# Kernel optimization log

Hardware: AMD Instinct MI355X
Metric: run time of the kernel (lower is better)

## Reference

```python
import jax, jax.numpy as jnp
import numpy as np

B, C, W, H = 1024, 1, 128, 128
NUM_IDS = 64
MARGIN = 0.3


def setup_inputs() -> dict:
    key = jax.random.key(0)
    k1, k2 = jax.random.split(key)
    inputs = jax.random.normal(k1, (B, C, W, H), dtype=jnp.float32)
    targets = jax.random.randint(k2, (B,), 0, NUM_IDS, dtype=jnp.int32)
    return {"inputs": inputs, "targets": targets}


def _dc_align(anchor, other):
    # Batched cross-attention alignment (DCModuleOptimized assumption):
    # modi = softmax(anchor @ other^T / sqrt(h)) @ other, per sample.
    h = anchor.shape[-1]
    scale = 1.0 / jnp.sqrt(jnp.asarray(h, anchor.dtype))
    att = jax.nn.softmax(jnp.einsum('bij,bkj->bik', anchor, other) * scale, axis=-1)
    return jnp.einsum('bik,bkj->bij', att, other)


def reference(inputs, targets):
    b, c, w, h = inputs.shape
    x = inputs.reshape(b, -1)                      # (n, d); requires c == 1 downstream
    n = b
    # Pairwise Euclidean distances, stable clamp as in torch code
    sq = jnp.sum(x * x, axis=1)                    # (n,)
    dist = sq[:, None] + sq[None, :] - 2.0 * (x @ x.T)
    dist = jnp.sqrt(jnp.clip(dist, 1e-12, None))   # (n, n)
    mask = targets[:, None] == targets[None, :]    # (n, n) same-identity mask
    # Vectorized hard mining (replaces the per-row Python loop)
    NEG = jnp.asarray(-1e30, dist.dtype)
    POS = jnp.asarray(1e30, dist.dtype)
    hp_idx = jnp.argmax(jnp.where(mask, dist, NEG), axis=1)   # hardest positive per row
    hn_idx = jnp.argmin(jnp.where(mask, POS, dist), axis=1)   # hardest negative per row
    anchor = x.reshape(b, w, h)
    h_pos = anchor[hp_idx]                         # (b, w, h) gathered hard positives
    h_neg = anchor[hn_idx]                         # (b, w, h) gathered hard negatives
    # DC module applied over the whole batch at once
    modi_pos = _dc_align(anchor, h_pos)
    modi_neg = _dc_align(anchor, h_neg)
    dap = anchor.reshape(b, -1) - modi_pos.reshape(b, -1)
    dan = anchor.reshape(b, -1) - modi_neg.reshape(b, -1)
    dist_ap = jnp.sqrt(jnp.sum(dap * dap, axis=1))
    dist_an = jnp.sqrt(jnp.sum(dan * dan, axis=1))
    # MarginRankingLoss with y = 1: mean(relu(dist_ap - dist_an + margin))
    loss = jnp.mean(jax.nn.relu(dist_ap - dist_an + MARGIN))
    return loss
```

## Files before the change

kernel.cpp:

```cpp
#include <hip/hip_runtime.h>
#include <stdint.h>

#define NSAMP 1024
#define D 16384
#define WH 128
#define MARGIN 0.3f
#define SCALE 0.08838834764831845f
#define RSCALE 11.313708498984761f
#define MARG 0.03f
#define NKS 16
#define NTILE 36

typedef unsigned int uint;
typedef unsigned short ushort_t;

typedef __attribute__((ext_vector_type(8))) short bf16x8;
typedef __attribute__((ext_vector_type(4))) float f32x4;

__device__ __forceinline__ float bf2f(unsigned short b) {
    return __uint_as_float(((uint)b) << 16);
}
__device__ __forceinline__ unsigned short f2bf(float f) {
    uint u = __float_as_uint(f);
    u += 0x7fffu + ((u >> 16) & 1u);
    return (unsigned short)(u >> 16);
}
__device__ __forceinline__ void gload_lds16(const void* g, void* l) {
    __builtin_amdgcn_global_load_lds(
        (const __attribute__((address_space(1))) uint32_t*)g,
        (__attribute__((address_space(3))) uint32_t*)l, 16, 0, 0);
}
__device__ __forceinline__ int lds_off(int row, int col) {
    return row * 256 + ((((col >> 3) ^ (row & 15)) << 4) | ((col & 7) << 1));
}

__global__ __launch_bounds__(256) void k_norms_hi(const float* __restrict__ x,
                                                  float* __restrict__ sq,
                                                  ushort_t* __restrict__ xhi) {
    int b = blockIdx.x;
    int tid = threadIdx.x;
    const float* xr = x + (size_t)b * D;
    ushort_t* hr = xhi + (size_t)b * D;
    float s = 0.f;
    #pragma unroll
    for (int m = 0; m < 16; ++m) {
        int e = m * 1024 + tid * 4;
        float4 v = *(const float4*)(xr + e);
        s += v.x * v.x + v.y * v.y + v.z * v.z + v.w * v.w;
        ushort4 h;
        h.x = f2bf(v.x); h.y = f2bf(v.y); h.z = f2bf(v.z); h.w = f2bf(v.w);
        *(ushort4*)(hr + e) = h;
    }
    for (int off = 32; off; off >>= 1) s += __shfl_down(s, off, 64);
    __shared__ float red[4];
    if ((tid & 63) == 0) red[tid >> 6] = s;
    __syncthreads();
    if (tid == 0) sq[b] = red[0] + red[1] + red[2] + red[3];
}

__global__ __launch_bounds__(256) void k_gram_hi(const ushort_t* __restrict__ xhi,
                                                 float* __restrict__ Gp) {
    int ks = blockIdx.x;
    int t = blockIdx.y;
    int bi = 0, rem = t;
    while (rem >= 8 - bi) { rem -= 8 - bi; ++bi; }
    int bj = bi + rem;
    int i0 = bi * 128, j0 = bj * 128;
    int kstart = ks * (D / NKS);

    int tid = threadIdx.x;
    int w = tid >> 6, lane = tid & 63;
    int wm = w & 1, wn = w >> 1;
    int quad = lane >> 4, m16 = lane & 15;
    int srow = lane >> 2, sseg = lane & 3;
    int swseg = sseg ^ ((srow >> 1) & 3);
    int rsw = (quad ^ ((m16 >> 1) & 3)) << 3;

    __shared__ __align__(16) ushort_t A_s[2][128 * 32];
    __shared__ __align__(16) ushort_t B_s[2][128 * 32];

    f32x4 acc[4][4];
    #pragma unroll
    for (int ii = 0; ii < 4; ++ii)
        #pragma unroll
        for (int jj = 0; jj < 4; ++jj)
            acc[ii][jj] = (f32x4){0.f, 0.f, 0.f, 0.f};

    const size_t Abase = (size_t)i0 * D;
    const size_t Bbase = (size_t)j0 * D;

    auto stage = [&](int bsel, int k0) {
        #pragma unroll
        for (int c = 0; c < 2; ++c) {
            int r = w * 32 + c * 16 + srow;
            size_t go = (size_t)r * D + k0 + swseg * 8;
            int lo = (w * 32 + c * 16) * 32;
            gload_lds16(xhi + Abase + go, &A_s[bsel][lo]);
            gload_lds16(xhi + Bbase + go, &B_s[bsel][lo]);
        }
    };

    stage(0, kstart);
    __syncthreads();
    int buf = 0;
    const int niter = (D / NKS) / 32;
    for (int kb = 0; kb < niter; ++kb) {
        if (kb < niter - 1) stage(buf ^ 1, kstart + (kb + 1) * 32);
        bf16x8 ah[4], bh[4];
        #pragma unroll
        for (int ii = 0; ii < 4; ++ii) {
            int ar = wm * 64 + ii * 16 + m16;
            ah[ii] = *(const bf16x8*)&A_s[buf][ar * 32 + rsw];
        }
        #pragma unroll
        for (int jj = 0; jj < 4; ++jj) {
            int br = wn * 64 + jj * 16 + m16;
            bh[jj] = *(const bf16x8*)&B_s[buf][br * 32 + rsw];
        }
        #pragma unroll
        for (int ii = 0; ii < 4; ++ii)
            #pragma unroll
            for (int jj = 0; jj < 4; ++jj)
                acc[ii][jj] = __builtin_amdgcn_mfma_f32_16x16x32_bf16(ah[ii], bh[jj], acc[ii][jj], 0, 0, 0);
        __syncthreads();
        buf ^= 1;
    }

    float* Gb = Gp + ((size_t)(t * NKS + ks) << 14);
    #pragma unroll
    for (int ii = 0; ii < 4; ++ii)
        #pragma unroll
        for (int jj = 0; jj < 4; ++jj) {
            int rg = wm * 64 + ii * 16 + quad * 4;
            int cg = wn * 64 + jj * 16 + m16;
            #pragma unroll
            for (int r = 0; r < 4; ++r)
                Gb[(rg + r) * 128 + cg] = acc[ii][jj][r];
        }
}

__global__ __launch_bounds__(256) void k_fold_tri(const float* __restrict__ Gp,
                                                  float* __restrict__ G) {
    int t = blockIdx.x;
    int panel = blockIdx.y;
    int bi = 0, rem = t;
    while (rem >= 8 - bi) { rem -= 8 - bi; ++bi; }
    int bj = bi + rem;
    bool diag = (bi == bj);
    int tid = threadIdx.x;

    const float* P = Gp + (((size_t)t * NKS) << 14) + panel * 4096;

    float4 s[4];
    #pragma unroll
    for (int m = 0; m < 4; ++m)
        s[m] = *(const float4*)(P + (tid + 256 * m) * 4);
    #pragma unroll
    for (int p = 1; p < NKS; ++p) {
        const float* Pp = P + (((size_t)p) << 14);
        #pragma unroll
        for (int m = 0; m < 4; ++m) {
            float4 v = *(const float4*)(Pp + (tid + 256 * m) * 4);
            s[m].x += v.x; s[m].y += v.y; s[m].z += v.z; s[m].w += v.w;
        }
    }

    int i0 = bi * 128, j0 = bj * 128, r0 = panel * 32;
    __shared__ float ts[32][129];
    #pragma unroll
    for (int m = 0; m < 4; ++m) {
        int p4 = (tid + 256 * m) * 4;
        int lr = p4 >> 7, lc = p4 & 127;
        *(float4*)(&G[(size_t)(i0 + r0 + lr) * NSAMP + j0 + lc]) = s[m];
        if (!diag) {
            ts[lr][lc] = s[m].x; ts[lr][lc + 1] = s[m].y;
            ts[lr][lc + 2] = s[m].z; ts[lr][lc + 3] = s[m].w;
        }
    }
    if (diag) return;
    __syncthreads();
    int oc = tid >> 1, half = tid & 1;
    float4 o[4];
    #pragma unroll
    for (int k = 0; k < 4; ++k) {
        int rr = half * 16 + k * 4;
        o[k].x = ts[rr][oc]; o[k].y = ts[rr + 1][oc];
        o[k].z = ts[rr + 2][oc]; o[k].w = ts[rr + 3][oc];
    }
    float* Gm = &G[(size_t)(j0 + oc) * NSAMP + i0 + r0 + half * 16];
    #pragma unroll
    for (int k = 0; k < 4; ++k) *(float4*)(Gm + k * 4) = o[k];
}

__global__ __launch_bounds__(256) void k_select_fix(const float* __restrict__ G,
                                                    const float* __restrict__ sq,
                                                    const int* __restrict__ tgt,
                                                    const float* __restrict__ x,
                                                    const ushort_t* __restrict__ xhi,
                                                    int* __restrict__ hp,
                                                    int* __restrict__ hn,
                                                    float* __restrict__ dsq) {
    int i = blockIdx.x;
    int tid = threadIdx.x;
    float sqi = sq[i];
    int ti = tgt[i];
    float dloc[4]; bool sloc[4];
    float pv = -3.0e38f; int pj = 0x7FFFFFFF;
    float nv = 3.0e38f;  int nj = 0x7FFFFFFF;
    #pragma unroll
    for (int m = 0; m < 4; ++m) {
        int j = tid + 256 * m;
        float g = G[(size_t)i * NSAMP + j];
        float d = sqrtf(fmaxf(sqi + sq[j] - 2.f * g, 1e-12f));
        bool same = (tgt[j] == ti);
        dloc[m] = d; sloc[m] = same;
        float cp = same ? d : -1e30f;
        float cn = same ? 1e30f : d;
        if (cp > pv || (cp == pv && j < pj)) { pv = cp; pj = j; }
        if (cn < nv || (cn == nv && j < nj)) { nv = cn; nj = j; }
    }
    for (int off = 32; off; off >>= 1) {
        float opv = __shfl_down(pv, off, 64); int opj = __shfl_down(pj, off, 64);
        float onv = __shfl_down(nv, off, 64); int onj = __shfl_down(nj, off, 64);
        if (opv > pv || (opv == pv && opj < pj)) { pv = opv; pj = opj; }
        if (onv < nv || (onv == nv && onj < nj)) { nv = onv; nj = onj; }
    }
    __shared__ float spv[4], snv[4];
    __shared__ int spj[4], snj[4];
    __shared__ float bb[2];
    __shared__ int cc[2];
    if ((tid & 63) == 0) { int wv = tid >> 6; spv[wv] = pv; spj[wv] = pj; snv[wv] = nv; snj[wv] = nj; }
    __syncthreads();
    if (tid == 0) {
        for (int wv = 1; wv < 4; ++wv) {
            if (spv[wv] > pv || (spv[wv] == pv && spj[wv] < pj)) { pv = spv[wv]; pj = spj[wv]; }
            if (snv[wv] < nv || (snv[wv] == nv && snj[wv] < nj)) { nv = snv[wv]; nj = snj[wv]; }
        }
        hp[i] = pj; hn[i] = nj;
        dsq[i] = sqi; dsq[NSAMP + i] = sqi;
        bb[0] = pv; bb[1] = nv;
        cc[0] = 0; cc[1] = 0;
    }
    __syncthreads();
    {
        int lp = 0, ln = 0;
        #pragma unroll
        for (int m = 0; m < 4; ++m) {
            if (sloc[m] && dloc[m] >= bb[0] - MARG) lp++;
            if (!sloc[m] && dloc[m] <= bb[1] + MARG) ln++;
        }
        if (lp) atomicAdd(&cc[0], lp);
        if (ln) atomicAdd(&cc[1], ln);
    }
    __syncthreads();

    __shared__ int cand[32];
    __shared__ int ncand;
    __shared__ float bred[4];
    const float* xi = x + (size_t)i * D;
    const ushort_t* hi = xhi + (size_t)i * D;
    for (int type = 0; type < 2; ++type) {
        if (cc[type] <= 1) continue;
        if (tid == 0) ncand = 0;
        __syncthreads();
        float bd = bb[type];
        #pragma unroll
        for (int m = 0; m < 4; ++m) {
            int j = tid + 256 * m;
            bool fl = (type == 0) ? (sloc[m] && dloc[m] >= bd - MARG)
                                  : (!sloc[m] && dloc[m] <= bd + MARG);
            if (fl) { int k = atomicAdd(&ncand, 1); if (k < 32) cand[k] = j; }
        }
        __syncthreads();
        int nc = ncand < 32 ? ncand : 32;
        float bestv = (type == 0) ? -3.0e38f : 3.0e38f;
        int bestj = 0x7FFFFFFF;
        for (int c = 0; c < nc; ++c) {
            int j = cand[c];
            const float* xj = x + (size_t)j * D;
            const ushort_t* hj = xhi + (size_t)j * D;
            float corr = 0.f;
            #pragma unroll
            for (int m = 0; m < 16; ++m) {
                int k = m * 1024 + tid * 4;
                float4 xa = *(const float4*)(xi + k);
                float4 xb = *(const float4*)(xj + k);
                ushort4 ha = *(const ushort4*)(hi + k);
                ushort4 hb = *(const ushort4*)(hj + k);
                float a0 = bf2f(ha.x), a1 = bf2f(ha.y), a2 = bf2f(ha.z), a3 = bf2f(ha.w);
                float b0 = bf2f(hb.x), b1 = bf2f(hb.y), b2 = bf2f(hb.z), b3 = bf2f(hb.w);
                corr += a0 * (xb.x - b0) + (xa.x - a0) * b0;
                corr += a1 * (xb.y - b1) + (xa.y - a1) * b1;
                corr += a2 * (xb.z - b2) + (xa.z - a2) * b2;
                corr += a3 * (xb.w - b3) + (xa.w - a3) * b3;
            }
            for (int off = 32; off; off >>= 1) corr += __shfl_down(corr, off, 64);
            if ((tid & 63) == 0) bred[tid >> 6] = corr;
            __syncthreads();
            float cs = bred[0] + bred[1] + bred[2] + bred[3];
            float g = G[(size_t)i * NSAMP + j];
            float d2 = sqi + sq[j] - 2.f * (g + cs);
            float d = sqrtf(fmaxf(d2, 1e-12f));
            if (type == 0) {
                if (d > bestv || (d == bestv && j < bestj)) { bestv = d; bestj = j; }
            } else {
                if (d < bestv || (d == bestv && j < bestj)) { bestv = d; bestj = j; }
            }
            __syncthreads();
        }
        if (tid == 0 && nc > 0) { if (type == 0) hp[i] = bestj; else hn[i] = bestj; }
        __syncthreads();
    }
}

__global__ __launch_bounds__(256) void k_dc_mfma(const ushort_t* __restrict__ xhi,
                                                 const int* __restrict__ hp,
                                                 const int* __restrict__ hn,
                                                 float* __restrict__ dsq) {
    int b = blockIdx.x;
    int which = blockIdx.y;
    int q = blockIdx.z;
    int oidx = (which == 0) ? hp[b] : hn[b];
    const ushort_t* Ag = xhi + (size_t)b * D;
    const ushort_t* Og = xhi + (size_t)oidx * D;

    __shared__ __align__(16) char smem[32768];

    int tid = threadIdx.x;
    int wv = tid >> 6, lane = tid & 63;
    int quad = lane >> 4, m16 = lane & 15;
    int rt = q * 4 + wv;

    bf16x8 af[4];
    #pragma unroll
    for (int ks = 0; ks < 4; ++ks)
        af[ks] = *(const bf16x8*)(Ag + (rt * 16 + m16) * WH + ks * 32 + quad * 8);

    {
        uint4 stg[8];
        #pragma unroll
        for (int k = 0; k < 8; ++k)
            stg[k] = *(const uint4*)((const char*)Og + (size_t)(tid + 256 * k) * 16);
        #pragma unroll
        for (int k = 0; k < 8; ++k) {
            int g = tid + 256 * k;
            *(uint4*)(smem + lds_off(g >> 4, (g & 15) * 8)) = stg[k];
        }
    }
    __syncthreads();

    f32x4 acc[8];
    #pragma unroll
    for (int ti = 0; ti < 8; ++ti)
        acc[ti] = (f32x4){0.f, 0.f, 0.f, 0.f};
    #pragma unroll
    for (int ks = 0; ks < 4; ++ks) {
        bf16x8 of[8];
        #pragma unroll
        for (int ti = 0; ti < 8; ++ti)
            of[ti] = *(const bf16x8*)(smem + lds_off(ti * 16 + m16, (ks * 4 + quad) * 8));
        #pragma unroll
        for (int ti = 0; ti < 8; ++ti)
            acc[ti] = __builtin_amdgcn_mfma_f32_16x16x32_bf16(of[ti], af[ks], acc[ti], 0, 0, 0);
    }

    int c0 = (tid & 31) * 4, h0 = (tid >> 5) * 16;
    uint4 trd[4][2];
    #pragma unroll
    for (int j = 0; j < 4; ++j)
        #pragma unroll
        for (int k = 0; k < 2; ++k)
            trd[j][k] = *(const uint4*)(smem + lds_off(c0 + j, h0 + 8 * k));
    __syncthreads();

    #pragma unroll
    for (int i = 0; i < 16; ++i) {
        uint v[4];
        #pragma unroll
        for (int j = 0; j < 4; ++j) {
            uint wo = ((const uint*)&trd[j][i >> 3])[(i >> 1) & 3];
            v[j] = (i & 1) ? (wo >> 16) : (wo & 0xffffu);
        }
        uint2 pk;
        pk.x = v[0] | (v[1] << 16);
        pk.y = v[2] | (v[3] << 16);
        *(uint2*)(smem + lds_off(h0 + i, c0)) = pk;
    }

    float tpart = 0.f;
    bf16x8 pf[4];
    {
        float mx = -3.0e38f;
        #pragma unroll
        for (int ti = 0; ti < 8; ++ti)
            #pragma unroll
            for (int r = 0; r < 4; ++r) {
                float s = acc[ti][r] * SCALE;
                acc[ti][r] = s;
                mx = fmaxf(mx, s);
            }
        mx = fmaxf(mx, __shfl_xor(mx, 16, 64));
        mx = fmaxf(mx, __shfl_xor(mx, 32, 64));
        float sum = 0.f, tnum = 0.f;
        #pragma unroll
        for (int ti = 0; ti < 8; ++ti)
            #pragma unroll
            for (int r = 0; r < 4; ++r) {
                float s = acc[ti][r];
                float e = __expf(s - mx);
                acc[ti][r] = e;
                sum += e;
                tnum += s * e;
            }
        sum += __shfl_xor(sum, 16, 64);
        sum += __shfl_xor(sum, 32, 64);
        tnum += __shfl_xor(tnum, 16, 64);
        tnum += __shfl_xor(tnum, 32, 64);
        float inv = 1.f / sum;
        tpart = 0.25f * tnum * inv;

        uint Ep[8][2];
        #pragma unroll
        for (int ti = 0; ti < 8; ++ti) {
            Ep[ti][0] = (uint)f2bf(acc[ti][0] * inv) |
                        ((uint)f2bf(acc[ti][1] * inv) << 16);
            Ep[ti][1] = (uint)f2bf(acc[ti][2] * inv) |
                        ((uint)f2bf(acc[ti][3] * inv) << 16);
        }
        int tih = quad >> 1;
        #pragma unroll
        for (int ks = 0; ks < 4; ++ks) {
            union { uint u[4]; bf16x8 v; } fr;
            #pragma unroll
            for (int k = 0; k < 4; ++k) {
                int src = (((quad << 1) + (k >> 1)) & 3) * 16 + m16;
                int a = __shfl((int)Ep[2 * ks + 0][k & 1], src, 64);
                int bsh = __shfl((int)Ep[2 * ks + 1][k & 1], src, 64);
                fr.u[k] = (uint)((tih == 0) ? a : bsh);
            }
            pf[ks] = fr.v;
        }
    }
    __syncthreads();

    #pragma unroll
    for (int tj = 0; tj < 8; ++tj)
        acc[tj] = (f32x4){0.f, 0.f, 0.f, 0.f};
    #pragma unroll
    for (int ks = 0; ks < 4; ++ks) {
        bf16x8 otf[8];
        #pragma unroll
        for (int tj = 0; tj < 8; ++tj)
            otf[tj] = *(const bf16x8*)(smem + lds_off(tj * 16 + m16, (ks * 4 + quad) * 8));
        #pragma unroll
        for (int tj = 0; tj < 8; ++tj)
            acc[tj] = __builtin_amdgcn_mfma_f32_16x16x32_bf16(pf[ks], otf[tj], acc[tj], 0, 0, 0);
    }

    float m2 = 0.f;
    #pragma unroll
    for (int tj = 0; tj < 8; ++tj)
        #pragma unroll
        for (int r = 0; r < 4; ++r) {
            float mvv = acc[tj][r];
            m2 += mvv * mvv;
        }
    float part = m2 - 2.f * RSCALE * tpart;
    for (int off = 32; off; off >>= 1) part += __shfl_down(part, off, 64);
    if (lane == 0) atomicAdd(&dsq[which * NSAMP + b], part);
}

__global__ void k_loss(const float* __restrict__ dsq, float* __restrict__ out) {
    int tid = threadIdx.x;
    float s = 0.f;
    #pragma unroll
    for (int m = 0; m < 4; ++m) {
        int b = tid + 256 * m;
        float ap = sqrtf(fmaxf(dsq[b], 0.f));
        float an = sqrtf(fmaxf(dsq[NSAMP + b], 0.f));
        s += fmaxf(ap - an + MARGIN, 0.f);
    }
    for (int off = 32; off; off >>= 1) s += __shfl_down(s, off, 64);
    __shared__ float red[4];
    if ((tid & 63) == 0) red[tid >> 6] = s;
    __syncthreads();
    if (tid == 0) out[0] = (red[0] + red[1] + red[2] + red[3]) * (1.f / NSAMP);
}

extern "C" void kernel_launch(void* const* d_in, const int* in_sizes, int n_in,
                              void* d_out, int out_size, void* d_ws, size_t ws_size,
                              hipStream_t stream) {
    const float* x = (const float*)d_in[0];
    const int* tgt = (const int*)d_in[1];
    float* out = (float*)d_out;
    char* ws = (char*)d_ws;

    const size_t GPB = (size_t)NTILE * NKS * 65536;
    const size_t XB = (size_t)NSAMP * D * 2;
    const size_t GB1 = (size_t)NSAMP * NSAMP * 4;

    float* Gp = (float*)ws;
    ushort_t* xhi = (ushort_t*)(ws + GPB);
    float* G = (float*)(ws + GPB + XB);
    char* tail = ws + GPB + XB + GB1;
    float* sq = (float*)tail;
    float* dsq = sq + NSAMP;
    int* hp = (int*)(dsq + 2 * NSAMP);
    int* hn = hp + NSAMP;

    k_norms_hi<<<NSAMP, 256, 0, stream>>>(x, sq, xhi);
    k_gram_hi<<<dim3(NKS, NTILE), 256, 0, stream>>>(xhi, Gp);
    k_fold_tri<<<dim3(NTILE, 4), 256, 0, stream>>>(Gp, G);
    k_select_fix<<<NSAMP, 256, 0, stream>>>(G, sq, tgt, x, xhi, hp, hn, dsq);
    k_dc_mfma<<<dim3(NSAMP, 2, 2), 256, 0, stream>>>(xhi, hp, hn, dsq);
    k_loss<<<1, 256, 0, stream>>>(dsq, out);
}
```

Before: 196.2 us.

## Deepen gram K-loop pipeline to four LDS stages and merge DC row halves

```diff
diff --git a/kernel.cpp b/kernel.cpp
--- a/kernel.cpp
+++ b/kernel.cpp
@@ -76,8 +76,8 @@
     int swseg = sseg ^ ((srow >> 1) & 3);
     int rsw = (quad ^ ((m16 >> 1) & 3)) << 3;
 
-    __shared__ __align__(16) ushort_t A_s[2][128 * 32];
-    __shared__ __align__(16) ushort_t B_s[2][128 * 32];
+    __shared__ __align__(16) ushort_t A_s[4][128 * 32];
+    __shared__ __align__(16) ushort_t B_s[4][128 * 32];
 
     f32x4 acc[4][4];
     #pragma unroll
@@ -89,7 +89,9 @@
     const size_t Abase = (size_t)i0 * D;
     const size_t Bbase = (size_t)j0 * D;
 
-    auto stage = [&](int bsel, int k0) {
+    auto stage = [&](int s) {
+        int bsel = s & 3;
+        int k0 = kstart + s * 32;
         #pragma unroll
         for (int c = 0; c < 2; ++c) {
             int r = w * 32 + c * 16 + srow;
@@ -99,32 +101,41 @@
             gload_lds16(xhi + Bbase + go, &B_s[bsel][lo]);
         }
     };
-
-    stage(0, kstart);
-    __syncthreads();
-    int buf = 0;
-    const int niter = (D / NKS) / 32;
-    for (int kb = 0; kb < niter; ++kb) {
-        if (kb < niter - 1) stage(buf ^ 1, kstart + (kb + 1) * 32);
+    auto compute = [&](int bsel) {
         bf16x8 ah[4], bh[4];
         #pragma unroll
         for (int ii = 0; ii < 4; ++ii) {
             int ar = wm * 64 + ii * 16 + m16;
-            ah[ii] = *(const bf16x8*)&A_s[buf][ar * 32 + rsw];
+            ah[ii] = *(const bf16x8*)&A_s[bsel][ar * 32 + rsw];
         }
         #pragma unroll
         for (int jj = 0; jj < 4; ++jj) {
             int br = wn * 64 + jj * 16 + m16;
-            bh[jj] = *(const bf16x8*)&B_s[buf][br * 32 + rsw];
+            bh[jj] = *(const bf16x8*)&B_s[bsel][br * 32 + rsw];
         }
         #pragma unroll
         for (int ii = 0; ii < 4; ++ii)
             #pragma unroll
             for (int jj = 0; jj < 4; ++jj)
                 acc[ii][jj] = __builtin_amdgcn_mfma_f32_16x16x32_bf16(ah[ii], bh[jj], acc[ii][jj], 0, 0, 0);
-        __syncthreads();
-        buf ^= 1;
-    }
+    };
+
+    stage(0); stage(1); stage(2);
+    for (int kb = 0; kb < 30; ++kb) {
+        asm volatile("s_waitcnt vmcnt(8)" ::: "memory");
+        __builtin_amdgcn_sched_barrier(0);
+        __builtin_amdgcn_s_barrier();
+        if (kb < 29) stage(kb + 3);
+        compute(kb & 3);
+    }
+    asm volatile("s_waitcnt vmcnt(4)" ::: "memory");
+    __builtin_amdgcn_sched_barrier(0);
+    __builtin_amdgcn_s_barrier();
+    compute(30 & 3);
+    asm volatile("s_waitcnt vmcnt(0)" ::: "memory");
+    __builtin_amdgcn_sched_barrier(0);
+    __builtin_amdgcn_s_barrier();
+    compute(31 & 3);
 
     float* Gb = Gp + ((size_t)(t * NKS + ks) << 14);
     #pragma unroll
@@ -319,7 +330,6 @@
                                                  float* __restrict__ dsq) {
     int b = blockIdx.x;
     int which = blockIdx.y;
-    int q = blockIdx.z;
     int oidx = (which == 0) ? hp[b] : hn[b];
     const ushort_t* Ag = xhi + (size_t)b * D;
     const ushort_t* Og = xhi + (size_t)oidx * D;
@@ -329,12 +339,15 @@
     int tid = threadIdx.x;
     int wv = tid >> 6, lane = tid & 63;
     int quad = lane >> 4, m16 = lane & 15;
-    int rt = q * 4 + wv;
-
-    bf16x8 af[4];
-    #pragma unroll
-    for (int ks = 0; ks < 4; ++ks)
-        af[ks] = *(const bf16x8*)(Ag + (rt * 16 + m16) * WH + ks * 32 + quad * 8);
+
+    bf16x8 af[2][4];
+    #pragma unroll
+    for (int h = 0; h < 2; ++h) {
+        int rt = h * 4 + wv;
+        #pragma unroll
+        for (int ks = 0; ks < 4; ++ks)
+            af[h][ks] = *(const bf16x8*)(Ag + (rt * 16 + m16) * WH + ks * 32 + quad * 8);
+    }
 
     {
         uint4 stg[8];
@@ -349,10 +362,12 @@
     }
     __syncthreads();
 
-    f32x4 acc[8];
-    #pragma unroll
-    for (int ti = 0; ti < 8; ++ti)
-        acc[ti] = (f32x4){0.f, 0.f, 0.f, 0.f};
+    f32x4 acc[2][8];
+    #pragma unroll
+    for (int h = 0; h < 2; ++h)
+        #pragma unroll
+        for (int ti = 0; ti < 8; ++ti)
+            acc[h][ti] = (f32x4){0.f, 0.f, 0.f, 0.f};
     #pragma unroll
     for (int ks = 0; ks < 4; ++ks) {
         bf16x8 of[8];
@@ -360,8 +375,10 @@
         for (int ti = 0; ti < 8; ++ti)
             of[ti] = *(const bf16x8*)(smem + lds_off(ti * 16 + m16, (ks * 4 + quad) * 8));
         #pragma unroll
-        for (int ti = 0; ti < 8; ++ti)
-            acc[ti] = __builtin_amdgcn_mfma_f32_16x16x32_bf16(of[ti], af[ks], acc[ti], 0, 0, 0);
+        for (int h = 0; h < 2; ++h)
+            #pragma unroll
+            for (int ti = 0; ti < 8; ++ti)
+                acc[h][ti] = __builtin_amdgcn_mfma_f32_16x16x32_bf16(of[ti], af[h][ks], acc[h][ti], 0, 0, 0);
     }
 
     int c0 = (tid & 31) * 4, h0 = (tid >> 5) * 16;
@@ -387,16 +404,17 @@
         *(uint2*)(smem + lds_off(h0 + i, c0)) = pk;
     }
 
-    float tpart = 0.f;
-    bf16x8 pf[4];
-    {
+    float tpart[2];
+    bf16x8 pf[2][4];
+    #pragma unroll
+    for (int h = 0; h < 2; ++h) {
         float mx = -3.0e38f;
         #pragma unroll
         for (int ti = 0; ti < 8; ++ti)
             #pragma unroll
             for (int r = 0; r < 4; ++r) {
-                float s = acc[ti][r] * SCALE;
-                acc[ti][r] = s;
+                float s = acc[h][ti][r] * SCALE;
+                acc[h][ti][r] = s;
                 mx = fmaxf(mx, s);
             }
         mx = fmaxf(mx, __shfl_xor(mx, 16, 64));
@@ -406,9 +424,9 @@
         for (int ti = 0; ti < 8; ++ti)
             #pragma unroll
             for (int r = 0; r < 4; ++r) {
-                float s = acc[ti][r];
+                float s = acc[h][ti][r];
                 float e = __expf(s - mx);
-                acc[ti][r] = e;
+                acc[h][ti][r] = e;
                 sum += e;
                 tnum += s * e;
             }
@@ -417,15 +435,15 @@
         tnum += __shfl_xor(tnum, 16, 64);
         tnum += __shfl_xor(tnum, 32, 64);
         float inv = 1.f / sum;
-        tpart = 0.25f * tnum * inv;
+        tpart[h] = 0.25f * tnum * inv;
 
         uint Ep[8][2];
         #pragma unroll
         for (int ti = 0; ti < 8; ++ti) {
-            Ep[ti][0] = (uint)f2bf(acc[ti][0] * inv) |
-                        ((uint)f2bf(acc[ti][1] * inv) << 16);
-            Ep[ti][1] = (uint)f2bf(acc[ti][2] * inv) |
-                        ((uint)f2bf(acc[ti][3] * inv) << 16);
+            Ep[ti][0] = (uint)f2bf(acc[h][ti][0] * inv) |
+                        ((uint)f2bf(acc[h][ti][1] * inv) << 16);
+            Ep[ti][1] = (uint)f2bf(acc[h][ti][2] * inv) |
+                        ((uint)f2bf(acc[h][ti][3] * inv) << 16);
         }
         int tih = quad >> 1;
         #pragma unroll
@@ -438,14 +456,16 @@
                 int bsh = __shfl((int)Ep[2 * ks + 1][k & 1], src, 64);
                 fr.u[k] = (uint)((tih == 0) ? a : bsh);
             }
-            pf[ks] = fr.v;
-        }
-    }
-    __syncthreads();
-
-    #pragma unroll
-    for (int tj = 0; tj < 8; ++tj)
-        acc[tj] = (f32x4){0.f, 0.f, 0.f, 0.f};
+            pf[h][ks] = fr.v;
+        }
+    }
+    __syncthreads();
+
+    #pragma unroll
+    for (int h = 0; h < 2; ++h)
+        #pragma unroll
+        for (int tj = 0; tj < 8; ++tj)
+            acc[h][tj] = (f32x4){0.f, 0.f, 0.f, 0.f};
     #pragma unroll
     for (int ks = 0; ks < 4; ++ks) {
         bf16x8 otf[8];
@@ -453,19 +473,25 @@
         for (int tj = 0; tj < 8; ++tj)
             otf[tj] = *(const bf16x8*)(smem + lds_off(tj * 16 + m16, (ks * 4 + quad) * 8));
         #pragma unroll
+        for (int h = 0; h < 2; ++h)
+            #pragma unroll
+            for (int tj = 0; tj < 8; ++tj)
+                acc[h][tj] = __builtin_amdgcn_mfma_f32_16x16x32_bf16(pf[h][ks], otf[tj], acc[h][tj], 0, 0, 0);
+    }
+
+    float part = 0.f;
+    #pragma unroll
+    for (int h = 0; h < 2; ++h) {
+        float m2 = 0.f;
+        #pragma unroll
         for (int tj = 0; tj < 8; ++tj)
-            acc[tj] = __builtin_amdgcn_mfma_f32_16x16x32_bf16(pf[ks], otf[tj], acc[tj], 0, 0, 0);
-    }
-
-    float m2 = 0.f;
-    #pragma unroll
-    for (int tj = 0; tj < 8; ++tj)
-        #pragma unroll
-        for (int r = 0; r < 4; ++r) {
-            float mvv = acc[tj][r];
-            m2 += mvv * mvv;
-        }
-    float part = m2 - 2.f * RSCALE * tpart;
+            #pragma unroll
+            for (int r = 0; r < 4; ++r) {
+                float mvv = acc[h][tj][r];
+                m2 += mvv * mvv;
+            }
+        part += m2 - 2.f * RSCALE * tpart[h];
+    }
     for (int off = 32; off; off >>= 1) part += __shfl_down(part, off, 64);
     if (lane == 0) atomicAdd(&dsq[which * NSAMP + b], part);
 }
@@ -512,6 +538,6 @@
     k_gram_hi<<<dim3(NKS, NTILE), 256, 0, stream>>>(xhi, Gp);
     k_fold_tri<<<dim3(NTILE, 4), 256, 0, stream>>>(Gp, G);
     k_select_fix<<<NSAMP, 256, 0, stream>>>(G, sq, tgt, x, xhi, hp, hn, dsq);
-    k_dc_mfma<<<dim3(NSAMP, 2, 2), 256, 0, stream>>>(xhi, hp, hn, dsq);
+    k_dc_mfma<<<dim3(NSAMP, 2), 256, 0, stream>>>(xhi, hp, hn, dsq);
     k_loss<<<1, 256, 0, stream>>>(dsq, out);
 }
```

Measured after the change: 200.6 us. 2.3% more time.

## Merge DC row-tile blocks, stage via direct LDS loads, remap gram grid, add setprio

Applied to the files above, without the earlier changes.

```diff
diff --git a/kernel.cpp b/kernel.cpp
--- a/kernel.cpp
+++ b/kernel.cpp
@@ -60,8 +60,12 @@
 
 __global__ __launch_bounds__(256) void k_gram_hi(const ushort_t* __restrict__ xhi,
                                                  float* __restrict__ Gp) {
-    int ks = blockIdx.x;
-    int t = blockIdx.y;
+    int n = blockIdx.x;
+    int r8 = n & 7;
+    int m = n >> 3;
+    int h = m / 36;
+    int t = m - 36 * h;
+    int ks = r8 + 8 * h;
     int bi = 0, rem = t;
     while (rem >= 8 - bi) { rem -= 8 - bi; ++bi; }
     int bj = bi + rem;
@@ -99,29 +103,33 @@
             gload_lds16(xhi + Bbase + go, &B_s[bsel][lo]);
         }
     };
-
-    stage(0, kstart);
-    __syncthreads();
-    int buf = 0;
-    const int niter = (D / NKS) / 32;
-    for (int kb = 0; kb < niter; ++kb) {
-        if (kb < niter - 1) stage(buf ^ 1, kstart + (kb + 1) * 32);
+    auto compute = [&](int bsel) {
         bf16x8 ah[4], bh[4];
         #pragma unroll
         for (int ii = 0; ii < 4; ++ii) {
             int ar = wm * 64 + ii * 16 + m16;
-            ah[ii] = *(const bf16x8*)&A_s[buf][ar * 32 + rsw];
+            ah[ii] = *(const bf16x8*)&A_s[bsel][ar * 32 + rsw];
         }
         #pragma unroll
         for (int jj = 0; jj < 4; ++jj) {
             int br = wn * 64 + jj * 16 + m16;
-            bh[jj] = *(const bf16x8*)&B_s[buf][br * 32 + rsw];
-        }
+            bh[jj] = *(const bf16x8*)&B_s[bsel][br * 32 + rsw];
+        }
+        __builtin_amdgcn_s_setprio(1);
         #pragma unroll
         for (int ii = 0; ii < 4; ++ii)
             #pragma unroll
             for (int jj = 0; jj < 4; ++jj)
                 acc[ii][jj] = __builtin_amdgcn_mfma_f32_16x16x32_bf16(ah[ii], bh[jj], acc[ii][jj], 0, 0, 0);
+        __builtin_amdgcn_s_setprio(0);
+    };
+
+    stage(0, kstart);
+    __syncthreads();
+    int buf = 0;
+    for (int kb = 0; kb < 32; ++kb) {
+        if (kb < 31) stage(buf ^ 1, kstart + (kb + 1) * 32);
+        compute(buf);
         __syncthreads();
         buf ^= 1;
     }
@@ -313,13 +321,12 @@
     }
 }
 
-__global__ __launch_bounds__(256) void k_dc_mfma(const ushort_t* __restrict__ xhi,
+__global__ __launch_bounds__(512) void k_dc_mfma(const ushort_t* __restrict__ xhi,
                                                  const int* __restrict__ hp,
                                                  const int* __restrict__ hn,
                                                  float* __restrict__ dsq) {
     int b = blockIdx.x;
     int which = blockIdx.y;
-    int q = blockIdx.z;
     int oidx = (which == 0) ? hp[b] : hn[b];
     const ushort_t* Ag = xhi + (size_t)b * D;
     const ushort_t* Og = xhi + (size_t)oidx * D;
@@ -329,24 +336,18 @@
     int tid = threadIdx.x;
     int wv = tid >> 6, lane = tid & 63;
     int quad = lane >> 4, m16 = lane & 15;
-    int rt = q * 4 + wv;
+
+    #pragma unroll
+    for (int k = 0; k < 4; ++k) {
+        int p = tid + 512 * k;
+        int row = p >> 4, s = p & 15;
+        gload_lds16(Og + row * 128 + ((s ^ (row & 15)) << 3), smem + p * 16);
+    }
 
     bf16x8 af[4];
     #pragma unroll
     for (int ks = 0; ks < 4; ++ks)
-        af[ks] = *(const bf16x8*)(Ag + (rt * 16 + m16) * WH + ks * 32 + quad * 8);
-
-    {
-        uint4 stg[8];
-        #pragma unroll
-        for (int k = 0; k < 8; ++k)
-            stg[k] = *(const uint4*)((const char*)Og + (size_t)(tid + 256 * k) * 16);
-        #pragma unroll
-        for (int k = 0; k < 8; ++k) {
-            int g = tid + 256 * k;
-            *(uint4*)(smem + lds_off(g >> 4, (g & 15) * 8)) = stg[k];
-        }
-    }
+        af[ks] = *(const bf16x8*)(Ag + (wv * 16 + m16) * WH + ks * 32 + quad * 8);
     __syncthreads();
 
     f32x4 acc[8];
@@ -359,26 +360,26 @@
         #pragma unroll
         for (int ti = 0; ti < 8; ++ti)
             of[ti] = *(const bf16x8*)(smem + lds_off(ti * 16 + m16, (ks * 4 + quad) * 8));
+        __builtin_amdgcn_s_setprio(1);
         #pragma unroll
         for (int ti = 0; ti < 8; ++ti)
             acc[ti] = __builtin_amdgcn_mfma_f32_16x16x32_bf16(of[ti], af[ks], acc[ti], 0, 0, 0);
-    }
-
-    int c0 = (tid & 31) * 4, h0 = (tid >> 5) * 16;
-    uint4 trd[4][2];
+        __builtin_amdgcn_s_setprio(0);
+    }
+
+    int c0 = (tid & 31) * 4, h0 = (tid >> 5) * 8;
+    uint4 trd[4];
     #pragma unroll
     for (int j = 0; j < 4; ++j)
-        #pragma unroll
-        for (int k = 0; k < 2; ++k)
-            trd[j][k] = *(const uint4*)(smem + lds_off(c0 + j, h0 + 8 * k));
-    __syncthreads();
-
-    #pragma unroll
-    for (int i = 0; i < 16; ++i) {
+        trd[j] = *(const uint4*)(smem + lds_off(c0 + j, h0));
+    __syncthreads();
+
+    #pragma unroll
+    for (int i = 0; i < 8; ++i) {
         uint v[4];
         #pragma unroll
         for (int j = 0; j < 4; ++j) {
-            uint wo = ((const uint*)&trd[j][i >> 3])[(i >> 1) & 3];
+            uint wo = ((const uint*)&trd[j])[i >> 1];
             v[j] = (i & 1) ? (wo >> 16) : (wo & 0xffffu);
         }
         uint2 pk;
@@ -387,7 +388,7 @@
         *(uint2*)(smem + lds_off(h0 + i, c0)) = pk;
     }
 
-    float tpart = 0.f;
+    float tpart;
     bf16x8 pf[4];
     {
         float mx = -3.0e38f;
@@ -452,9 +453,11 @@
         #pragma unroll
         for (int tj = 0; tj < 8; ++tj)
             otf[tj] = *(const bf16x8*)(smem + lds_off(tj * 16 + m16, (ks * 4 + quad) * 8));
+        __builtin_amdgcn_s_setprio(1);
         #pragma unroll
         for (int tj = 0; tj < 8; ++tj)
             acc[tj] = __builtin_amdgcn_mfma_f32_16x16x32_bf16(pf[ks], otf[tj], acc[tj], 0, 0, 0);
+        __builtin_amdgcn_s_setprio(0);
     }
 
     float m2 = 0.f;
@@ -509,9 +512,9 @@
     int* hn = hp + NSAMP;
 
     k_norms_hi<<<NSAMP, 256, 0, stream>>>(x, sq, xhi);
-    k_gram_hi<<<dim3(NKS, NTILE), 256, 0, stream>>>(xhi, Gp);
+    k_gram_hi<<<NKS * NTILE, 256, 0, stream>>>(xhi, Gp);
     k_fold_tri<<<dim3(NTILE, 4), 256, 0, stream>>>(Gp, G);
     k_select_fix<<<NSAMP, 256, 0, stream>>>(G, sq, tgt, x, xhi, hp, hn, dsq);
-    k_dc_mfma<<<dim3(NSAMP, 2, 2), 256, 0, stream>>>(xhi, hp, hn, dsq);
+    k_dc_mfma<<<dim3(NSAMP, 2), 512, 0, stream>>>(xhi, hp, hn, dsq);
     k_loss<<<1, 256, 0, stream>>>(dsq, out);
 }
```

Result: faster. 192.3 us (median of 2 runs) (-2.0%).
